# Kernel optimization log

Measured on AMD Instinct MI355X. Metric: run time of the kernel, lower is better.

Reference implementation:

```python
import jax, jax.numpy as jnp
import numpy as np

BAND_WIDTH = 0.05
EPS = 1e-5
NORM_EPS = 1e-12  # F.normalize clamp_min


def _l2_normalize_channels(x):
    # x: (B, C, D, H, W); normalize over channel dim=1 like F.normalize(p=2, dim=1)
    n = jnp.sqrt(jnp.sum(x * x, axis=1, keepdims=True))
    return x / jnp.maximum(n, NORM_EPS)


def setup_inputs() -> dict:
    key = jax.random.key(0)
    k1, k2, k3 = jax.random.split(key, 3)
    B, C, D, H, W = 2, 256, 8, 8, 8
    P, K = 128, 512  # n_patches iterations, k=512 sampled voxels per patch
    S = D * H * W  # 512 spatial voxels
    t2_feat = jax.random.normal(k1, (B, C, D, H, W), dtype=jnp.float32)
    t1_feat = jax.random.normal(k2, (B, C, D, H, W), dtype=jnp.float32)
    idx = jax.random.randint(k3, (P, K), 0, S, dtype=jnp.int32)
    return {"t2_feat": t2_feat, "t1_feat": t1_feat, "idx": idx}


def reference(t2_feat, t1_feat, idx):
    B, C = t2_feat.shape[:2]
    # normalize channels, flatten spatial dims: (B, C, S)
    t2 = _l2_normalize_channels(t2_feat).reshape(B, C, -1)
    t1 = _l2_normalize_channels(t1_feat).reshape(B, C, -1)
    # gather the same random voxels for both modalities: (B, C, P, K)
    t2p = t2[:, :, idx]
    t1p = t1[:, :, idx]
    # batched cosine similarity: bmm(t2p^T, t1p) per patch -> (P, B, K, K)
    cs = jnp.einsum('bcpk,bcpl->pbkl', t2p, t1p)
    e = jnp.exp(cs / BAND_WIDTH)
    pos = jnp.diagonal(e, axis1=2, axis2=3)  # (P, B, K) exp of positives
    # InfoNCE over columns (torch dim=1 of (B,K,K)) and rows (dim=2)
    info_nce1 = pos / jnp.sum(e, axis=2)
    info_nce2 = pos / jnp.sum(e, axis=3)
    info_nce = 0.5 * (info_nce1 + info_nce2)
    # per-patch mean of -log, then mean over patches == global mean
    return jnp.mean(-jnp.log(info_nce + EPS))
```

## Files before the change

kernel.cpp:

```cpp
#include <hip/hip_runtime.h>

typedef __attribute__((ext_vector_type(8))) short bf16x8;
typedef __attribute__((ext_vector_type(4))) float f32x4;
typedef __attribute__((ext_vector_type(4))) ushort u16x4;

#define C_DIM 256
#define S_DIM 512
#define P_DIM 128
#define K_DIM 512
#define INV_BW 20.0f
#define EPS_LOSS 1e-5f

#define OFF_SS2    0
#define OFF_SS1    1024
#define OFF_DIAG   2048
#define OFF_CNTBF  3072
#define OFF_T2BF   35840
#define OFF_T1BF   166912
#define OFF_EBF    297984
#define OFF_ETBF   560128
#define OFF_D1P    35840
#define OFF_D2P    822272
#define OFF_PART   1084416
#define OFF_TICKET 1084544

__device__ inline ushort f2bf(float f) {
  union { float f; uint u; } v; v.f = f;
  return (ushort)((v.u + 0x7FFF + ((v.u >> 16) & 1)) >> 16);
}

#define TP 260
__global__ __launch_bounds__(256) void pre_kernel(
    const float* __restrict__ t2, const float* __restrict__ t1,
    const int* __restrict__ idx,
    float* __restrict__ ss2, float* __restrict__ ss1,
    ushort* __restrict__ t2bfT, ushort* __restrict__ t1bfT,
    ushort* __restrict__ cntbf, int* __restrict__ ticket) {
  int blk = blockIdx.x, tid = threadIdx.x;
  if (blk < 64) {
    __shared__ ushort tl[16][TP];
    __shared__ float ps[16][17];
    int b = blk >> 5, stile = blk & 31;
    int s0 = stile * 16;
    int ls = tid & 15, cg = tid >> 4;
    int wv = tid >> 6, ln = tid & 63;
    #pragma unroll
    for (int tt = 0; tt < 2; ++tt) {
      const float* src = (tt ? t1 : t2) + b * (C_DIM * S_DIM);
      ushort* dst = (tt ? t1bfT : t2bfT) + b * (S_DIM * C_DIM);
      float a = 0.f;
      #pragma unroll
      for (int k = 0; k < 16; ++k) {
        int c = cg + 16 * k;
        float v = src[c * S_DIM + s0 + ls];
        a += v * v;
        tl[ls][c] = f2bf(v);
      }
      ps[cg][ls] = a;
      __syncthreads();
      if (tid < 16) {
        float ss = 0.f;
        #pragma unroll
        for (int j = 0; j < 16; ++j) ss += ps[j][tid];
        (tt ? ss1 : ss2)[b * S_DIM + s0 + tid] = ss;
      }
      #pragma unroll
      for (int i = 0; i < 4; ++i) {
        int sl = wv * 4 + i;
        u16x4 pk = *reinterpret_cast<const u16x4*>(&tl[sl][ln * 4]);
        *reinterpret_cast<u16x4*>(&dst[(s0 + sl) * C_DIM + ln * 4]) = pk;
      }
      __syncthreads();
    }
  } else {
    __shared__ int c_lds[S_DIM];
    int p = blk - 64;
    if (blk == 64 && tid == 0) *ticket = 0;
    c_lds[tid] = 0; c_lds[tid + 256] = 0;
    __syncthreads();
    atomicAdd(&c_lds[idx[p * K_DIM + tid]], 1);
    atomicAdd(&c_lds[idx[p * K_DIM + tid + 256]], 1);
    __syncthreads();
    cntbf[p * S_DIM + tid]       = f2bf((float)c_lds[tid]);
    cntbf[p * S_DIM + tid + 256] = f2bf((float)c_lds[tid + 256]);
  }
}

__global__ __launch_bounds__(256) void gemm_exp_mfma_kernel(
    const ushort* __restrict__ t2bfT, const ushort* __restrict__ t1bfT,
    const float* __restrict__ ss2, const float* __restrict__ ss1,
    ushort* __restrict__ Ebf, ushort* __restrict__ ETbf,
    float* __restrict__ diag) {
  int wave = threadIdx.x >> 6, lane = threadIdx.x & 63;
  int job = blockIdx.x * 4 + wave;
  int n = job & 31, m = (job >> 5) & 31, b = job >> 10;
  int m0 = m * 16, c0 = n * 16;
  int lr = lane & 15, lo = lane >> 4;
  const ushort* ap = t2bfT + b * (S_DIM * C_DIM) + (m0 + lr) * C_DIM + lo * 8;
  const ushort* bp = t1bfT + b * (S_DIM * C_DIM) + (c0 + lr) * C_DIM + lo * 8;
  f32x4 acc = {0.f, 0.f, 0.f, 0.f};
  #pragma unroll
  for (int k = 0; k < 8; ++k) {
    bf16x8 af = *reinterpret_cast<const bf16x8*>(ap + k * 32);
    bf16x8 bv = *reinterpret_cast<const bf16x8*>(bp + k * 32);
    acc = __builtin_amdgcn_mfma_f32_16x16x32_bf16(af, bv, acc, 0, 0, 0);
  }
  float bs = 1.0f / fmaxf(sqrtf(ss1[b * S_DIM + c0 + lr]), 1e-12f);
  float e[4]; ushort eb[4];
  ushort* Eb  = Ebf  + b * (S_DIM * S_DIM);
  ushort* ETb = ETbf + b * (S_DIM * S_DIM);
  #pragma unroll
  for (int r = 0; r < 4; ++r) {
    int row = m0 + lo * 4 + r;
    float as = 1.0f / fmaxf(sqrtf(ss2[b * S_DIM + row]), 1e-12f);
    e[r] = expf(acc[r] * as * bs * INV_BW);
    eb[r] = f2bf(e[r]);
    Eb[row * S_DIM + c0 + lr] = eb[r];
  }
  u16x4 pk = {eb[0], eb[1], eb[2], eb[3]};
  *reinterpret_cast<u16x4*>(&ETb[(c0 + lr) * S_DIM + m0 + lo * 4]) = pk;
  if (m == n && (lr >> 2) == lo) diag[b * S_DIM + m0 + lr] = e[lr & 3];
}

__global__ __launch_bounds__(256) void denom_mfma_kernel(
    const ushort* __restrict__ Ebf, const ushort* __restrict__ ETbf,
    const ushort* __restrict__ cntbf,
    float* __restrict__ D1p, float* __restrict__ D2p) {
  int wave = threadIdx.x >> 6, lane = threadIdx.x & 63;
  int job = blockIdx.x * 4 + wave;
  int n = job & 31, m = (job >> 5) & 7, b = (job >> 8) & 1;
  int z = (job >> 9) & 1, h = job >> 10;
  int m0 = m * 16, col0 = n * 16;
  const ushort* Bmat = (z ? Ebf : ETbf) + b * (S_DIM * S_DIM);
  float* Dp = (z ? D2p : D1p) + h * (P_DIM * 2 * S_DIM);
  int lr = lane & 15, lo = lane >> 4;
  const ushort* aptr = cntbf + (m0 + lr) * S_DIM + h * 256 + lo * 8;
  const ushort* bptr = Bmat + (col0 + lr) * S_DIM + h * 256 + lo * 8;
  f32x4 acc = {0.f, 0.f, 0.f, 0.f};
  #pragma unroll
  for (int k = 0; k < 8; ++k) {
    bf16x8 af = *reinterpret_cast<const bf16x8*>(aptr + k * 32);
    bf16x8 bv = *reinterpret_cast<const bf16x8*>(bptr + k * 32);
    acc = __builtin_amdgcn_mfma_f32_16x16x32_bf16(af, bv, acc, 0, 0, 0);
  }
  #pragma unroll
  for (int r = 0; r < 4; ++r) {
    int p = m0 + lo * 4 + r;
    Dp[(p * 2 + b) * S_DIM + col0 + lr] = acc[r];
  }
}

__global__ __launch_bounds__(512) void loss_final_kernel(
    const int* __restrict__ idx, const float* __restrict__ diag,
    const float* __restrict__ D1p, const float* __restrict__ D2p,
    float* __restrict__ part, int* __restrict__ ticket, float* __restrict__ out) {
  const int HOFF = P_DIM * 2 * S_DIM;
  int p = blockIdx.x, k = threadIdx.x;
  int s = idx[p * K_DIM + k];
  float acc = 0.f;
  #pragma unroll
  for (int b = 0; b < 2; ++b) {
    float pos = diag[b * S_DIM + s];
    int o = (p * 2 + b) * S_DIM + s;
    float d1 = D1p[o] + D1p[HOFF + o];
    float d2 = D2p[o] + D2p[HOFF + o];
    acc += logf(0.5f * (pos / d1 + pos / d2) + EPS_LOSS);
  }
  for (int o = 32; o; o >>= 1) acc += __shfl_down(acc, o);
  __shared__ float red[8];
  __shared__ int lastflag;
  if ((k & 63) == 0) red[k >> 6] = acc;
  __syncthreads();
  if (k == 0) {
    float tsum = 0.f;
    #pragma unroll
    for (int i = 0; i < 8; ++i) tsum += red[i];
    atomicExch(&part[p], tsum);
    __threadfence();
    int old = atomicAdd(ticket, 1);
    lastflag = (old == P_DIM - 1);
  }
  __syncthreads();
  if (lastflag) {
    __threadfence();
    float v = (k < P_DIM) ? atomicAdd(&part[k], 0.0f) : 0.0f;
    for (int o = 32; o; o >>= 1) v += __shfl_down(v, o);
    __shared__ float red2[8];
    if ((k & 63) == 0) red2[k >> 6] = v;
    __syncthreads();
    if (k == 0) {
      float tsum = 0.f;
      #pragma unroll
      for (int i = 0; i < 8; ++i) tsum += red2[i];
      out[0] = -tsum * (1.0f / (P_DIM * 2.0f * K_DIM));
    }
  }
}

extern "C" void kernel_launch(void* const* d_in, const int* in_sizes, int n_in,
                              void* d_out, int out_size, void* d_ws, size_t ws_size,
                              hipStream_t stream) {
  const float* t2 = (const float*)d_in[0];
  const float* t1 = (const float*)d_in[1];
  const int* idx  = (const int*)d_in[2];
  float* ws = (float*)d_ws;
  float*  ss2    = ws + OFF_SS2;
  float*  ss1    = ws + OFF_SS1;
  float*  diag   = ws + OFF_DIAG;
  ushort* cntbf  = (ushort*)(ws + OFF_CNTBF);
  ushort* t2bfT  = (ushort*)(ws + OFF_T2BF);
  ushort* t1bfT  = (ushort*)(ws + OFF_T1BF);
  ushort* Ebf    = (ushort*)(ws + OFF_EBF);
  ushort* ETbf   = (ushort*)(ws + OFF_ETBF);
  float*  D1p    = ws + OFF_D1P;
  float*  D2p    = ws + OFF_D2P;
  float*  part   = ws + OFF_PART;
  int*    ticket = (int*)(ws + OFF_TICKET);

  pre_kernel<<<192, 256, 0, stream>>>(t2, t1, idx, ss2, ss1, t2bfT, t1bfT,
                                      cntbf, ticket);
  gemm_exp_mfma_kernel<<<512, 256, 0, stream>>>(t2bfT, t1bfT, ss2, ss1,
                                                Ebf, ETbf, diag);
  denom_mfma_kernel<<<512, 256, 0, stream>>>(Ebf, ETbf, cntbf, D1p, D2p);
  loss_final_kernel<<<P_DIM, 512, 0, stream>>>(idx, diag, D1p, D2p, part, ticket,
                                               (float*)d_out);
}
```

Baseline: 30.66 us.

## Fuse Gram/exp and count-weighted denominator GEMMs into one kernel via LDS

Merges the exp-Gram kernel and the denominator GEMM into a single kernel. Each block computes a 16-column strip of exp(similarity) for one side, holds it in LDS as bf16, then immediately multiplies it by the patch count matrix to produce full-K denominators. This removes the global round trip of the 512x512 E and E^T matrices, one kernel launch, and the half-split partial sums. The pre-kernel is also split so each block handles one tensor, doubling its parallelism. In exchange the fused kernel runs only 128 blocks with 512 threads, which may underfill the GPU, and each side recomputes its own Gram strip.

Measured after the change: 34.36 us. 1.12x slower.

```diff
diff --git a/kernel.cpp b/kernel.cpp
--- a/kernel.cpp
+++ b/kernel.cpp
@@ -17,12 +17,10 @@
 #define OFF_CNTBF  3072
 #define OFF_T2BF   35840
 #define OFF_T1BF   166912
-#define OFF_EBF    297984
-#define OFF_ETBF   560128
-#define OFF_D1P    35840
-#define OFF_D2P    822272
-#define OFF_PART   1084416
-#define OFF_TICKET 1084544
+#define OFF_D1     297984
+#define OFF_D2     429056
+#define OFF_PART   560128
+#define OFF_TICKET 560256
 
 __device__ inline ushort f2bf(float f) {
   union { float f; uint u; } v; v.f = f;
@@ -37,45 +35,42 @@
     ushort* __restrict__ t2bfT, ushort* __restrict__ t1bfT,
     ushort* __restrict__ cntbf, int* __restrict__ ticket) {
   int blk = blockIdx.x, tid = threadIdx.x;
-  if (blk < 64) {
+  if (blk < 128) {
     __shared__ ushort tl[16][TP];
     __shared__ float ps[16][17];
-    int b = blk >> 5, stile = blk & 31;
+    int tt = blk >> 6, b = (blk >> 5) & 1, stile = blk & 31;
     int s0 = stile * 16;
+    const float* src = (tt ? t1 : t2) + b * (C_DIM * S_DIM);
+    ushort* dst = (tt ? t1bfT : t2bfT) + b * (S_DIM * C_DIM);
+    float* ssd = (tt ? ss1 : ss2) + b * S_DIM;
     int ls = tid & 15, cg = tid >> 4;
+    float a = 0.f;
+    #pragma unroll
+    for (int k = 0; k < 16; ++k) {
+      int c = cg + 16 * k;
+      float v = src[c * S_DIM + s0 + ls];
+      a += v * v;
+      tl[ls][c] = f2bf(v);
+    }
+    ps[cg][ls] = a;
+    __syncthreads();
+    if (tid < 16) {
+      float ss = 0.f;
+      #pragma unroll
+      for (int j = 0; j < 16; ++j) ss += ps[j][tid];
+      ssd[s0 + tid] = ss;
+    }
     int wv = tid >> 6, ln = tid & 63;
     #pragma unroll
-    for (int tt = 0; tt < 2; ++tt) {
-      const float* src = (tt ? t1 : t2) + b * (C_DIM * S_DIM);
-      ushort* dst = (tt ? t1bfT : t2bfT) + b * (S_DIM * C_DIM);
-      float a = 0.f;
-      #pragma unroll
-      for (int k = 0; k < 16; ++k) {
-        int c = cg + 16 * k;
-        float v = src[c * S_DIM + s0 + ls];
-        a += v * v;
-        tl[ls][c] = f2bf(v);
-      }
-      ps[cg][ls] = a;
-      __syncthreads();
-      if (tid < 16) {
-        float ss = 0.f;
-        #pragma unroll
-        for (int j = 0; j < 16; ++j) ss += ps[j][tid];
-        (tt ? ss1 : ss2)[b * S_DIM + s0 + tid] = ss;
-      }
-      #pragma unroll
-      for (int i = 0; i < 4; ++i) {
-        int sl = wv * 4 + i;
-        u16x4 pk = *reinterpret_cast<const u16x4*>(&tl[sl][ln * 4]);
-        *reinterpret_cast<u16x4*>(&dst[(s0 + sl) * C_DIM + ln * 4]) = pk;
-      }
-      __syncthreads();
+    for (int i = 0; i < 4; ++i) {
+      int sl = wv * 4 + i;
+      u16x4 pk = *reinterpret_cast<const u16x4*>(&tl[sl][ln * 4]);
+      *reinterpret_cast<u16x4*>(&dst[(s0 + sl) * C_DIM + ln * 4]) = pk;
     }
   } else {
     __shared__ int c_lds[S_DIM];
-    int p = blk - 64;
-    if (blk == 64 && tid == 0) *ticket = 0;
+    int p = blk - 128;
+    if (blk == 128 && tid == 0) *ticket = 0;
     c_lds[tid] = 0; c_lds[tid + 256] = 0;
     __syncthreads();
     atomicAdd(&c_lds[idx[p * K_DIM + tid]], 1);
@@ -86,75 +81,71 @@
   }
 }
 
-__global__ __launch_bounds__(256) void gemm_exp_mfma_kernel(
+__global__ __launch_bounds__(512) void gram_denom_kernel(
     const ushort* __restrict__ t2bfT, const ushort* __restrict__ t1bfT,
     const float* __restrict__ ss2, const float* __restrict__ ss1,
-    ushort* __restrict__ Ebf, ushort* __restrict__ ETbf,
-    float* __restrict__ diag) {
+    const ushort* __restrict__ cntbf,
+    float* __restrict__ D1, float* __restrict__ D2, float* __restrict__ diag) {
+  __shared__ ushort ldsE[16][520];
+  int blk = blockIdx.x;
+  int side = blk >> 6, b = (blk >> 5) & 1, fb = blk & 31;
+  int f0 = fb * 16;
   int wave = threadIdx.x >> 6, lane = threadIdx.x & 63;
-  int job = blockIdx.x * 4 + wave;
-  int n = job & 31, m = (job >> 5) & 31, b = job >> 10;
-  int m0 = m * 16, c0 = n * 16;
   int lr = lane & 15, lo = lane >> 4;
-  const ushort* ap = t2bfT + b * (S_DIM * C_DIM) + (m0 + lr) * C_DIM + lo * 8;
-  const ushort* bp = t1bfT + b * (S_DIM * C_DIM) + (c0 + lr) * C_DIM + lo * 8;
+  const ushort* varMat = (side ? t1bfT : t2bfT) + b * (S_DIM * C_DIM);
+  const ushort* fixMat = (side ? t2bfT : t1bfT) + b * (S_DIM * C_DIM);
+  const float* vss = (side ? ss1 : ss2) + b * S_DIM;
+  const float* fss = (side ? ss2 : ss1) + b * S_DIM;
+  float fscale = 1.0f / fmaxf(sqrtf(fss[f0 + lr]), 1e-12f);
+  bf16x8 ffr[8];
+  #pragma unroll
+  for (int k = 0; k < 8; ++k)
+    ffr[k] = *reinterpret_cast<const bf16x8*>(
+        fixMat + (f0 + lr) * C_DIM + lo * 8 + k * 32);
+  #pragma unroll
+  for (int i = 0; i < 4; ++i) {
+    int v0 = (wave * 4 + i) * 16;
+    const ushort* ap = varMat + (v0 + lr) * C_DIM + lo * 8;
+    f32x4 acc = {0.f, 0.f, 0.f, 0.f};
+    #pragma unroll
+    for (int k = 0; k < 8; ++k) {
+      bf16x8 af = *reinterpret_cast<const bf16x8*>(ap + k * 32);
+      acc = __builtin_amdgcn_mfma_f32_16x16x32_bf16(af, ffr[k], acc, 0, 0, 0);
+    }
+    ushort eb[4];
+    #pragma unroll
+    for (int r = 0; r < 4; ++r) {
+      int vrow = v0 + lo * 4 + r;
+      float vs = 1.0f / fmaxf(sqrtf(vss[vrow]), 1e-12f);
+      float e = expf(acc[r] * vs * fscale * INV_BW);
+      eb[r] = f2bf(e);
+      if (side == 0 && vrow == f0 + lr) diag[b * S_DIM + vrow] = e;
+    }
+    u16x4 pk = {eb[0], eb[1], eb[2], eb[3]};
+    *reinterpret_cast<u16x4*>(&ldsE[lr][v0 + lo * 4]) = pk;
+  }
+  __syncthreads();
+  int p0 = wave * 16;
+  const ushort* cp = cntbf + (p0 + lr) * S_DIM + lo * 8;
   f32x4 acc = {0.f, 0.f, 0.f, 0.f};
   #pragma unroll
-  for (int k = 0; k < 8; ++k) {
-    bf16x8 af = *reinterpret_cast<const bf16x8*>(ap + k * 32);
-    bf16x8 bv = *reinterpret_cast<const bf16x8*>(bp + k * 32);
-    acc = __builtin_amdgcn_mfma_f32_16x16x32_bf16(af, bv, acc, 0, 0, 0);
-  }
-  float bs = 1.0f / fmaxf(sqrtf(ss1[b * S_DIM + c0 + lr]), 1e-12f);
-  float e[4]; ushort eb[4];
-  ushort* Eb  = Ebf  + b * (S_DIM * S_DIM);
-  ushort* ETb = ETbf + b * (S_DIM * S_DIM);
+  for (int k = 0; k < 16; ++k) {
+    bf16x8 af = *reinterpret_cast<const bf16x8*>(cp + k * 32);
+    bf16x8 bf_ = *reinterpret_cast<const bf16x8*>(&ldsE[lr][lo * 8 + k * 32]);
+    acc = __builtin_amdgcn_mfma_f32_16x16x32_bf16(af, bf_, acc, 0, 0, 0);
+  }
+  float* Dout = side ? D2 : D1;
   #pragma unroll
   for (int r = 0; r < 4; ++r) {
-    int row = m0 + lo * 4 + r;
-    float as = 1.0f / fmaxf(sqrtf(ss2[b * S_DIM + row]), 1e-12f);
-    e[r] = expf(acc[r] * as * bs * INV_BW);
-    eb[r] = f2bf(e[r]);
-    Eb[row * S_DIM + c0 + lr] = eb[r];
-  }
-  u16x4 pk = {eb[0], eb[1], eb[2], eb[3]};
-  *reinterpret_cast<u16x4*>(&ETb[(c0 + lr) * S_DIM + m0 + lo * 4]) = pk;
-  if (m == n && (lr >> 2) == lo) diag[b * S_DIM + m0 + lr] = e[lr & 3];
-}
-
-__global__ __launch_bounds__(256) void denom_mfma_kernel(
-    const ushort* __restrict__ Ebf, const ushort* __restrict__ ETbf,
-    const ushort* __restrict__ cntbf,
-    float* __restrict__ D1p, float* __restrict__ D2p) {
-  int wave = threadIdx.x >> 6, lane = threadIdx.x & 63;
-  int job = blockIdx.x * 4 + wave;
-  int n = job & 31, m = (job >> 5) & 7, b = (job >> 8) & 1;
-  int z = (job >> 9) & 1, h = job >> 10;
-  int m0 = m * 16, col0 = n * 16;
-  const ushort* Bmat = (z ? Ebf : ETbf) + b * (S_DIM * S_DIM);
-  float* Dp = (z ? D2p : D1p) + h * (P_DIM * 2 * S_DIM);
-  int lr = lane & 15, lo = lane >> 4;
-  const ushort* aptr = cntbf + (m0 + lr) * S_DIM + h * 256 + lo * 8;
-  const ushort* bptr = Bmat + (col0 + lr) * S_DIM + h * 256 + lo * 8;
-  f32x4 acc = {0.f, 0.f, 0.f, 0.f};
-  #pragma unroll
-  for (int k = 0; k < 8; ++k) {
-    bf16x8 af = *reinterpret_cast<const bf16x8*>(aptr + k * 32);
-    bf16x8 bv = *reinterpret_cast<const bf16x8*>(bptr + k * 32);
-    acc = __builtin_amdgcn_mfma_f32_16x16x32_bf16(af, bv, acc, 0, 0, 0);
-  }
-  #pragma unroll
-  for (int r = 0; r < 4; ++r) {
-    int p = m0 + lo * 4 + r;
-    Dp[(p * 2 + b) * S_DIM + col0 + lr] = acc[r];
+    int p = p0 + lo * 4 + r;
+    Dout[(p * 2 + b) * S_DIM + f0 + lr] = acc[r];
   }
 }
 
 __global__ __launch_bounds__(512) void loss_final_kernel(
     const int* __restrict__ idx, const float* __restrict__ diag,
-    const float* __restrict__ D1p, const float* __restrict__ D2p,
+    const float* __restrict__ D1, const float* __restrict__ D2,
     float* __restrict__ part, int* __restrict__ ticket, float* __restrict__ out) {
-  const int HOFF = P_DIM * 2 * S_DIM;
   int p = blockIdx.x, k = threadIdx.x;
   int s = idx[p * K_DIM + k];
   float acc = 0.f;
@@ -162,8 +153,8 @@
   for (int b = 0; b < 2; ++b) {
     float pos = diag[b * S_DIM + s];
     int o = (p * 2 + b) * S_DIM + s;
-    float d1 = D1p[o] + D1p[HOFF + o];
-    float d2 = D2p[o] + D2p[HOFF + o];
+    float d1 = D1[o];
+    float d2 = D2[o];
     acc += logf(0.5f * (pos / d1 + pos / d2) + EPS_LOSS);
   }
   for (int o = 32; o; o >>= 1) acc += __shfl_down(acc, o);
@@ -210,18 +201,15 @@
   ushort* cntbf  = (ushort*)(ws + OFF_CNTBF);
   ushort* t2bfT  = (ushort*)(ws + OFF_T2BF);
   ushort* t1bfT  = (ushort*)(ws + OFF_T1BF);
-  ushort* Ebf    = (ushort*)(ws + OFF_EBF);
-  ushort* ETbf   = (ushort*)(ws + OFF_ETBF);
-  float*  D1p    = ws + OFF_D1P;
-  float*  D2p    = ws + OFF_D2P;
+  float*  D1     = ws + OFF_D1;
+  float*  D2     = ws + OFF_D2;
   float*  part   = ws + OFF_PART;
   int*    ticket = (int*)(ws + OFF_TICKET);
 
-  pre_kernel<<<192, 256, 0, stream>>>(t2, t1, idx, ss2, ss1, t2bfT, t1bfT,
+  pre_kernel<<<256, 256, 0, stream>>>(t2, t1, idx, ss2, ss1, t2bfT, t1bfT,
                                       cntbf, ticket);
-  gemm_exp_mfma_kernel<<<512, 256, 0, stream>>>(t2bfT, t1bfT, ss2, ss1,
-                                                Ebf, ETbf, diag);
-  denom_mfma_kernel<<<512, 256, 0, stream>>>(Ebf, ETbf, cntbf, D1p, D2p);
-  loss_final_kernel<<<P_DIM, 512, 0, stream>>>(idx, diag, D1p, D2p, part, ticket,
+  gram_denom_kernel<<<128, 512, 0, stream>>>(t2bfT, t1bfT, ss2, ss1, cntbf,
+                                             D1, D2, diag);
+  loss_final_kernel<<<P_DIM, 512, 0, stream>>>(idx, diag, D1, D2, part, ticket,
                                                (float*)d_out);
 }
```

## Fuse gemm, denominator and loss kernels into one persistent kernel with grid barriers

Applied to the files above, without the earlier changes.

Merges the three post-processing kernels into a single 256-block, 512-thread kernel that separates the GEMM+exp, denominator GEMM and loss stages with software grid barriers built on agent-scope atomics. It also splits the pre-kernel so each block converts one tensor instead of two, giving 256 blocks. The aim is to remove two kernel launch gaps. The cost is spin-wait barriers that depend on all 256 blocks being co-resident, and D buffers moved to new workspace offsets.

Measured after the change: 54.08 us. 76.4% more time.

```diff
diff --git a/kernel.cpp b/kernel.cpp
--- a/kernel.cpp
+++ b/kernel.cpp
@@ -19,14 +19,26 @@
 #define OFF_T1BF   166912
 #define OFF_EBF    297984
 #define OFF_ETBF   560128
-#define OFF_D1P    35840
-#define OFF_D2P    822272
-#define OFF_PART   1084416
-#define OFF_TICKET 1084544
+#define OFF_D1     822272
+#define OFF_D2     1084416
+#define OFF_PART   1346560
+#define OFF_BAR    1346816
 
 __device__ inline ushort f2bf(float f) {
   union { float f; uint u; } v; v.f = f;
   return (ushort)((v.u + 0x7FFF + ((v.u >> 16) & 1)) >> 16);
+}
+
+__device__ inline void grid_barrier(int* c, int n) {
+  __syncthreads();
+  if (threadIdx.x == 0) {
+    __builtin_amdgcn_fence(__ATOMIC_RELEASE, "agent");
+    __hip_atomic_fetch_add(c, 1, __ATOMIC_RELAXED, __HIP_MEMORY_SCOPE_AGENT);
+    while (__hip_atomic_load(c, __ATOMIC_RELAXED, __HIP_MEMORY_SCOPE_AGENT) < n)
+      __builtin_amdgcn_s_sleep(2);
+    __builtin_amdgcn_fence(__ATOMIC_ACQUIRE, "agent");
+  }
+  __syncthreads();
 }
 
 #define TP 260
@@ -35,47 +47,44 @@
     const int* __restrict__ idx,
     float* __restrict__ ss2, float* __restrict__ ss1,
     ushort* __restrict__ t2bfT, ushort* __restrict__ t1bfT,
-    ushort* __restrict__ cntbf, int* __restrict__ ticket) {
+    ushort* __restrict__ cntbf, int* __restrict__ bar) {
   int blk = blockIdx.x, tid = threadIdx.x;
-  if (blk < 64) {
+  if (blk < 128) {
     __shared__ ushort tl[16][TP];
     __shared__ float ps[16][17];
-    int b = blk >> 5, stile = blk & 31;
+    int tt = blk >> 6, b = (blk >> 5) & 1, stile = blk & 31;
     int s0 = stile * 16;
+    const float* src = (tt ? t1 : t2) + b * (C_DIM * S_DIM);
+    ushort* dst = (tt ? t1bfT : t2bfT) + b * (S_DIM * C_DIM);
+    float* ssd = (tt ? ss1 : ss2) + b * S_DIM;
     int ls = tid & 15, cg = tid >> 4;
+    float a = 0.f;
+    #pragma unroll
+    for (int k = 0; k < 16; ++k) {
+      int c = cg + 16 * k;
+      float v = src[c * S_DIM + s0 + ls];
+      a += v * v;
+      tl[ls][c] = f2bf(v);
+    }
+    ps[cg][ls] = a;
+    __syncthreads();
+    if (tid < 16) {
+      float ss = 0.f;
+      #pragma unroll
+      for (int j = 0; j < 16; ++j) ss += ps[j][tid];
+      ssd[s0 + tid] = ss;
+    }
     int wv = tid >> 6, ln = tid & 63;
     #pragma unroll
-    for (int tt = 0; tt < 2; ++tt) {
-      const float* src = (tt ? t1 : t2) + b * (C_DIM * S_DIM);
-      ushort* dst = (tt ? t1bfT : t2bfT) + b * (S_DIM * C_DIM);
-      float a = 0.f;
-      #pragma unroll
-      for (int k = 0; k < 16; ++k) {
-        int c = cg + 16 * k;
-        float v = src[c * S_DIM + s0 + ls];
-        a += v * v;
-        tl[ls][c] = f2bf(v);
-      }
-      ps[cg][ls] = a;
-      __syncthreads();
-      if (tid < 16) {
-        float ss = 0.f;
-        #pragma unroll
-        for (int j = 0; j < 16; ++j) ss += ps[j][tid];
-        (tt ? ss1 : ss2)[b * S_DIM + s0 + tid] = ss;
-      }
-      #pragma unroll
-      for (int i = 0; i < 4; ++i) {
-        int sl = wv * 4 + i;
-        u16x4 pk = *reinterpret_cast<const u16x4*>(&tl[sl][ln * 4]);
-        *reinterpret_cast<u16x4*>(&dst[(s0 + sl) * C_DIM + ln * 4]) = pk;
-      }
-      __syncthreads();
+    for (int i = 0; i < 4; ++i) {
+      int sl = wv * 4 + i;
+      u16x4 pk = *reinterpret_cast<const u16x4*>(&tl[sl][ln * 4]);
+      *reinterpret_cast<u16x4*>(&dst[(s0 + sl) * C_DIM + ln * 4]) = pk;
     }
   } else {
     __shared__ int c_lds[S_DIM];
-    int p = blk - 64;
-    if (blk == 64 && tid == 0) *ticket = 0;
+    int p = blk - 128;
+    if (blk == 128 && tid < 3) bar[tid] = 0;
     c_lds[tid] = 0; c_lds[tid + 256] = 0;
     __syncthreads();
     atomicAdd(&c_lds[idx[p * K_DIM + tid]], 1);
@@ -86,113 +95,114 @@
   }
 }
 
-__global__ __launch_bounds__(256) void gemm_exp_mfma_kernel(
+__global__ __launch_bounds__(512) void fused_kernel(
     const ushort* __restrict__ t2bfT, const ushort* __restrict__ t1bfT,
     const float* __restrict__ ss2, const float* __restrict__ ss1,
+    const ushort* __restrict__ cntbf, const int* __restrict__ idx,
     ushort* __restrict__ Ebf, ushort* __restrict__ ETbf,
-    float* __restrict__ diag) {
-  int wave = threadIdx.x >> 6, lane = threadIdx.x & 63;
-  int job = blockIdx.x * 4 + wave;
-  int n = job & 31, m = (job >> 5) & 31, b = job >> 10;
-  int m0 = m * 16, c0 = n * 16;
+    float* __restrict__ D1, float* __restrict__ D2, float* __restrict__ diag,
+    float* __restrict__ part2, int* __restrict__ bar, float* __restrict__ out) {
+  int blk = blockIdx.x, tid = threadIdx.x;
+  int wave = tid >> 6, lane = tid & 63;
   int lr = lane & 15, lo = lane >> 4;
-  const ushort* ap = t2bfT + b * (S_DIM * C_DIM) + (m0 + lr) * C_DIM + lo * 8;
-  const ushort* bp = t1bfT + b * (S_DIM * C_DIM) + (c0 + lr) * C_DIM + lo * 8;
-  f32x4 acc = {0.f, 0.f, 0.f, 0.f};
-  #pragma unroll
-  for (int k = 0; k < 8; ++k) {
-    bf16x8 af = *reinterpret_cast<const bf16x8*>(ap + k * 32);
-    bf16x8 bv = *reinterpret_cast<const bf16x8*>(bp + k * 32);
-    acc = __builtin_amdgcn_mfma_f32_16x16x32_bf16(af, bv, acc, 0, 0, 0);
-  }
-  float bs = 1.0f / fmaxf(sqrtf(ss1[b * S_DIM + c0 + lr]), 1e-12f);
-  float e[4]; ushort eb[4];
-  ushort* Eb  = Ebf  + b * (S_DIM * S_DIM);
-  ushort* ETb = ETbf + b * (S_DIM * S_DIM);
-  #pragma unroll
-  for (int r = 0; r < 4; ++r) {
-    int row = m0 + lo * 4 + r;
-    float as = 1.0f / fmaxf(sqrtf(ss2[b * S_DIM + row]), 1e-12f);
-    e[r] = expf(acc[r] * as * bs * INV_BW);
-    eb[r] = f2bf(e[r]);
-    Eb[row * S_DIM + c0 + lr] = eb[r];
-  }
-  u16x4 pk = {eb[0], eb[1], eb[2], eb[3]};
-  *reinterpret_cast<u16x4*>(&ETb[(c0 + lr) * S_DIM + m0 + lo * 4]) = pk;
-  if (m == n && (lr >> 2) == lo) diag[b * S_DIM + m0 + lr] = e[lr & 3];
-}
-
-__global__ __launch_bounds__(256) void denom_mfma_kernel(
-    const ushort* __restrict__ Ebf, const ushort* __restrict__ ETbf,
-    const ushort* __restrict__ cntbf,
-    float* __restrict__ D1p, float* __restrict__ D2p) {
-  int wave = threadIdx.x >> 6, lane = threadIdx.x & 63;
-  int job = blockIdx.x * 4 + wave;
-  int n = job & 31, m = (job >> 5) & 7, b = (job >> 8) & 1;
-  int z = (job >> 9) & 1, h = job >> 10;
-  int m0 = m * 16, col0 = n * 16;
-  const ushort* Bmat = (z ? Ebf : ETbf) + b * (S_DIM * S_DIM);
-  float* Dp = (z ? D2p : D1p) + h * (P_DIM * 2 * S_DIM);
-  int lr = lane & 15, lo = lane >> 4;
-  const ushort* aptr = cntbf + (m0 + lr) * S_DIM + h * 256 + lo * 8;
-  const ushort* bptr = Bmat + (col0 + lr) * S_DIM + h * 256 + lo * 8;
-  f32x4 acc = {0.f, 0.f, 0.f, 0.f};
-  #pragma unroll
-  for (int k = 0; k < 8; ++k) {
-    bf16x8 af = *reinterpret_cast<const bf16x8*>(aptr + k * 32);
-    bf16x8 bv = *reinterpret_cast<const bf16x8*>(bptr + k * 32);
-    acc = __builtin_amdgcn_mfma_f32_16x16x32_bf16(af, bv, acc, 0, 0, 0);
-  }
-  #pragma unroll
-  for (int r = 0; r < 4; ++r) {
-    int p = m0 + lo * 4 + r;
-    Dp[(p * 2 + b) * S_DIM + col0 + lr] = acc[r];
-  }
-}
-
-__global__ __launch_bounds__(512) void loss_final_kernel(
-    const int* __restrict__ idx, const float* __restrict__ diag,
-    const float* __restrict__ D1p, const float* __restrict__ D2p,
-    float* __restrict__ part, int* __restrict__ ticket, float* __restrict__ out) {
-  const int HOFF = P_DIM * 2 * S_DIM;
-  int p = blockIdx.x, k = threadIdx.x;
-  int s = idx[p * K_DIM + k];
-  float acc = 0.f;
-  #pragma unroll
-  for (int b = 0; b < 2; ++b) {
+
+  {
+    int job = blk * 8 + wave;
+    int n = job & 31, m = (job >> 5) & 31, b = job >> 10;
+    int m0 = m * 16, c0 = n * 16;
+    const ushort* ap = t2bfT + b * (S_DIM * C_DIM) + (m0 + lr) * C_DIM + lo * 8;
+    const ushort* bp = t1bfT + b * (S_DIM * C_DIM) + (c0 + lr) * C_DIM + lo * 8;
+    f32x4 acc = {0.f, 0.f, 0.f, 0.f};
+    #pragma unroll
+    for (int k = 0; k < 8; ++k) {
+      bf16x8 af = *reinterpret_cast<const bf16x8*>(ap + k * 32);
+      bf16x8 bv = *reinterpret_cast<const bf16x8*>(bp + k * 32);
+      acc = __builtin_amdgcn_mfma_f32_16x16x32_bf16(af, bv, acc, 0, 0, 0);
+    }
+    float bs = 1.0f / fmaxf(sqrtf(ss1[b * S_DIM + c0 + lr]), 1e-12f);
+    float e[4]; ushort eb[4];
+    ushort* Eb  = Ebf  + b * (S_DIM * S_DIM);
+    ushort* ETb = ETbf + b * (S_DIM * S_DIM);
+    #pragma unroll
+    for (int r = 0; r < 4; ++r) {
+      int row = m0 + lo * 4 + r;
+      float as = 1.0f / fmaxf(sqrtf(ss2[b * S_DIM + row]), 1e-12f);
+      e[r] = expf(acc[r] * as * bs * INV_BW);
+      eb[r] = f2bf(e[r]);
+      Eb[row * S_DIM + c0 + lr] = eb[r];
+    }
+    u16x4 pk = {eb[0], eb[1], eb[2], eb[3]};
+    *reinterpret_cast<u16x4*>(&ETb[(c0 + lr) * S_DIM + m0 + lo * 4]) = pk;
+    if (m == n && (lr >> 2) == lo) diag[b * S_DIM + m0 + lr] = e[lr & 3];
+  }
+  grid_barrier(&bar[0], 256);
+
+  {
+    int job = blk * 8 + wave;
+    int n = job & 31, m = (job >> 5) & 7, b = (job >> 8) & 1;
+    int z = (job >> 9) & 1, h = job >> 10;
+    int m0 = m * 16, col0 = n * 16;
+    const ushort* Bmat = (z ? Ebf : ETbf) + b * (S_DIM * S_DIM);
+    const ushort* aptr = cntbf + (m0 + lr) * S_DIM + h * 256 + lo * 8;
+    const ushort* bptr = Bmat + (col0 + lr) * S_DIM + h * 256 + lo * 8;
+    f32x4 acc = {0.f, 0.f, 0.f, 0.f};
+    #pragma unroll
+    for (int k = 0; k < 8; ++k) {
+      bf16x8 af = *reinterpret_cast<const bf16x8*>(aptr + k * 32);
+      bf16x8 bv = *reinterpret_cast<const bf16x8*>(bptr + k * 32);
+      acc = __builtin_amdgcn_mfma_f32_16x16x32_bf16(af, bv, acc, 0, 0, 0);
+    }
+    float* Dp = (z ? D2 : D1);
+    #pragma unroll
+    for (int r = 0; r < 4; ++r) {
+      int p = m0 + lo * 4 + r;
+      Dp[((h * P_DIM + p) * 2 + b) * S_DIM + col0 + lr] = acc[r];
+    }
+  }
+  grid_barrier(&bar[1], 256);
+
+  {
+    const int HOFF = P_DIM * 2 * S_DIM;
+    int p = blk >> 1, kh = blk & 1;
+    int b = tid >> 8, kk = kh * 256 + (tid & 255);
+    int s = idx[p * K_DIM + kk];
     float pos = diag[b * S_DIM + s];
     int o = (p * 2 + b) * S_DIM + s;
-    float d1 = D1p[o] + D1p[HOFF + o];
-    float d2 = D2p[o] + D2p[HOFF + o];
-    acc += logf(0.5f * (pos / d1 + pos / d2) + EPS_LOSS);
-  }
-  for (int o = 32; o; o >>= 1) acc += __shfl_down(acc, o);
-  __shared__ float red[8];
-  __shared__ int lastflag;
-  if ((k & 63) == 0) red[k >> 6] = acc;
-  __syncthreads();
-  if (k == 0) {
-    float tsum = 0.f;
-    #pragma unroll
-    for (int i = 0; i < 8; ++i) tsum += red[i];
-    atomicExch(&part[p], tsum);
-    __threadfence();
-    int old = atomicAdd(ticket, 1);
-    lastflag = (old == P_DIM - 1);
-  }
-  __syncthreads();
-  if (lastflag) {
-    __threadfence();
-    float v = (k < P_DIM) ? atomicAdd(&part[k], 0.0f) : 0.0f;
-    for (int o = 32; o; o >>= 1) v += __shfl_down(v, o);
-    __shared__ float red2[8];
-    if ((k & 63) == 0) red2[k >> 6] = v;
-    __syncthreads();
-    if (k == 0) {
+    float d1 = D1[o] + D1[HOFF + o];
+    float d2 = D2[o] + D2[HOFF + o];
+    float term = logf(0.5f * (pos / d1 + pos / d2) + EPS_LOSS);
+    for (int off = 32; off; off >>= 1) term += __shfl_down(term, off);
+    __shared__ float red[8];
+    __shared__ int lastflag;
+    if (lane == 0) red[wave] = term;
+    __syncthreads();
+    if (tid == 0) {
       float tsum = 0.f;
       #pragma unroll
-      for (int i = 0; i < 8; ++i) tsum += red2[i];
-      out[0] = -tsum * (1.0f / (P_DIM * 2.0f * K_DIM));
+      for (int i = 0; i < 8; ++i) tsum += red[i];
+      atomicExch(&part2[blk], tsum);
+      __builtin_amdgcn_fence(__ATOMIC_RELEASE, "agent");
+      int old = __hip_atomic_fetch_add(&bar[2], 1, __ATOMIC_ACQ_REL,
+                                       __HIP_MEMORY_SCOPE_AGENT);
+      lastflag = (old == 255);
+    }
+    __syncthreads();
+    if (lastflag) {
+      if (tid == 0) __builtin_amdgcn_fence(__ATOMIC_ACQUIRE, "agent");
+      __syncthreads();
+      float v = (tid < 256)
+          ? __hip_atomic_load(&part2[tid], __ATOMIC_RELAXED,
+                              __HIP_MEMORY_SCOPE_AGENT) : 0.f;
+      for (int off = 32; off; off >>= 1) v += __shfl_down(v, off);
+      __shared__ float red2[8];
+      if (lane == 0) red2[wave] = v;
+      __syncthreads();
+      if (tid == 0) {
+        float tsum = 0.f;
+        #pragma unroll
+        for (int i = 0; i < 8; ++i) tsum += red2[i];
+        out[0] = -tsum * (1.0f / (P_DIM * 2.0f * K_DIM));
+      }
     }
   }
 }
@@ -212,16 +222,14 @@
   ushort* t1bfT  = (ushort*)(ws + OFF_T1BF);
   ushort* Ebf    = (ushort*)(ws + OFF_EBF);
   ushort* ETbf   = (ushort*)(ws + OFF_ETBF);
-  float*  D1p    = ws + OFF_D1P;
-  float*  D2p    = ws + OFF_D2P;
-  float*  part   = ws + OFF_PART;
-  int*    ticket = (int*)(ws + OFF_TICKET);
-
-  pre_kernel<<<192, 256, 0, stream>>>(t2, t1, idx, ss2, ss1, t2bfT, t1bfT,
-                                      cntbf, ticket);
-  gemm_exp_mfma_kernel<<<512, 256, 0, stream>>>(t2bfT, t1bfT, ss2, ss1,
-                                                Ebf, ETbf, diag);
-  denom_mfma_kernel<<<512, 256, 0, stream>>>(Ebf, ETbf, cntbf, D1p, D2p);
-  loss_final_kernel<<<P_DIM, 512, 0, stream>>>(idx, diag, D1p, D2p, part, ticket,
-                                               (float*)d_out);
-}
+  float*  D1     = ws + OFF_D1;
+  float*  D2     = ws + OFF_D2;
+  float*  part2  = ws + OFF_PART;
+  int*    bar    = (int*)(ws + OFF_BAR);
+
+  pre_kernel<<<256, 256, 0, stream>>>(t2, t1, idx, ss2, ss1, t2bfT, t1bfT,
+                                      cntbf, bar);
+  fused_kernel<<<256, 512, 0, stream>>>(t2bfT, t1bfT, ss2, ss1, cntbf, idx,
+                                        Ebf, ETbf, D1, D2, diag, part2, bar,
+                                        (float*)d_out);
+}
```

## Reuse MFMA operand fragments across two tiles per wave and split pre-kernel work

Applied to the files above, without the earlier changes.

Each wave in the GEMM-exp and denominator kernels now keeps one operand's fragments in registers and computes two 16x16 output tiles, halving those kernels' grid sizes and cutting redundant global loads. The pre-kernel splits the t2/t1 conversion across twice as many blocks instead of looping in one block. It also uses fast __expf/__logf intrinsics and moves the D1/D2 buffers to their own workspace region rather than overlapping the bf16 transposes. The trade-off is fewer waves available to hide latency and slightly lower precision from the fast math.

New measurement: 30.08 us. About the same (-1.9%).

```diff
diff --git a/kernel.cpp b/kernel.cpp
--- a/kernel.cpp
+++ b/kernel.cpp
@@ -19,10 +19,10 @@
 #define OFF_T1BF   166912
 #define OFF_EBF    297984
 #define OFF_ETBF   560128
-#define OFF_D1P    35840
-#define OFF_D2P    822272
-#define OFF_PART   1084416
-#define OFF_TICKET 1084544
+#define OFF_D1     822272
+#define OFF_D2     1084416
+#define OFF_PART   1346560
+#define OFF_BAR    1346816
 
 __device__ inline ushort f2bf(float f) {
   union { float f; uint u; } v; v.f = f;
@@ -35,47 +35,44 @@
     const int* __restrict__ idx,
     float* __restrict__ ss2, float* __restrict__ ss1,
     ushort* __restrict__ t2bfT, ushort* __restrict__ t1bfT,
-    ushort* __restrict__ cntbf, int* __restrict__ ticket) {
+    ushort* __restrict__ cntbf, int* __restrict__ bar) {
   int blk = blockIdx.x, tid = threadIdx.x;
-  if (blk < 64) {
+  if (blk < 128) {
     __shared__ ushort tl[16][TP];
     __shared__ float ps[16][17];
-    int b = blk >> 5, stile = blk & 31;
+    int tt = blk >> 6, b = (blk >> 5) & 1, stile = blk & 31;
     int s0 = stile * 16;
+    const float* src = (tt ? t1 : t2) + b * (C_DIM * S_DIM);
+    ushort* dst = (tt ? t1bfT : t2bfT) + b * (S_DIM * C_DIM);
+    float* ssd = (tt ? ss1 : ss2) + b * S_DIM;
     int ls = tid & 15, cg = tid >> 4;
+    float a = 0.f;
+    #pragma unroll
+    for (int k = 0; k < 16; ++k) {
+      int c = cg + 16 * k;
+      float v = src[c * S_DIM + s0 + ls];
+      a += v * v;
+      tl[ls][c] = f2bf(v);
+    }
+    ps[cg][ls] = a;
+    __syncthreads();
+    if (tid < 16) {
+      float ss = 0.f;
+      #pragma unroll
+      for (int j = 0; j < 16; ++j) ss += ps[j][tid];
+      ssd[s0 + tid] = ss;
+    }
     int wv = tid >> 6, ln = tid & 63;
     #pragma unroll
-    for (int tt = 0; tt < 2; ++tt) {
-      const float* src = (tt ? t1 : t2) + b * (C_DIM * S_DIM);
-      ushort* dst = (tt ? t1bfT : t2bfT) + b * (S_DIM * C_DIM);
-      float a = 0.f;
-      #pragma unroll
-      for (int k = 0; k < 16; ++k) {
-        int c = cg + 16 * k;
-        float v = src[c * S_DIM + s0 + ls];
-        a += v * v;
-        tl[ls][c] = f2bf(v);
-      }
-      ps[cg][ls] = a;
-      __syncthreads();
-      if (tid < 16) {
-        float ss = 0.f;
-        #pragma unroll
-        for (int j = 0; j < 16; ++j) ss += ps[j][tid];
-        (tt ? ss1 : ss2)[b * S_DIM + s0 + tid] = ss;
-      }
-      #pragma unroll
-      for (int i = 0; i < 4; ++i) {
-        int sl = wv * 4 + i;
-        u16x4 pk = *reinterpret_cast<const u16x4*>(&tl[sl][ln * 4]);
-        *reinterpret_cast<u16x4*>(&dst[(s0 + sl) * C_DIM + ln * 4]) = pk;
-      }
-      __syncthreads();
+    for (int i = 0; i < 4; ++i) {
+      int sl = wv * 4 + i;
+      u16x4 pk = *reinterpret_cast<const u16x4*>(&tl[sl][ln * 4]);
+      *reinterpret_cast<u16x4*>(&dst[(s0 + sl) * C_DIM + ln * 4]) = pk;
     }
   } else {
     __shared__ int c_lds[S_DIM];
-    int p = blk - 64;
-    if (blk == 64 && tid == 0) *ticket = 0;
+    int p = blk - 128;
+    if (blk == 128 && tid < 3) bar[tid] = 0;
     c_lds[tid] = 0; c_lds[tid + 256] = 0;
     __syncthreads();
     atomicAdd(&c_lds[idx[p * K_DIM + tid]], 1);
@@ -93,67 +90,82 @@
     float* __restrict__ diag) {
   int wave = threadIdx.x >> 6, lane = threadIdx.x & 63;
   int job = blockIdx.x * 4 + wave;
-  int n = job & 31, m = (job >> 5) & 31, b = job >> 10;
-  int m0 = m * 16, c0 = n * 16;
+  int n = job & 31, mp = (job >> 5) & 15, b = job >> 9;
+  int c0 = n * 16;
   int lr = lane & 15, lo = lane >> 4;
-  const ushort* ap = t2bfT + b * (S_DIM * C_DIM) + (m0 + lr) * C_DIM + lo * 8;
+  const ushort* base2 = t2bfT + b * (S_DIM * C_DIM);
   const ushort* bp = t1bfT + b * (S_DIM * C_DIM) + (c0 + lr) * C_DIM + lo * 8;
-  f32x4 acc = {0.f, 0.f, 0.f, 0.f};
-  #pragma unroll
-  for (int k = 0; k < 8; ++k) {
-    bf16x8 af = *reinterpret_cast<const bf16x8*>(ap + k * 32);
-    bf16x8 bv = *reinterpret_cast<const bf16x8*>(bp + k * 32);
-    acc = __builtin_amdgcn_mfma_f32_16x16x32_bf16(af, bv, acc, 0, 0, 0);
-  }
+  bf16x8 bfr[8];
+  #pragma unroll
+  for (int k = 0; k < 8; ++k)
+    bfr[k] = *reinterpret_cast<const bf16x8*>(bp + k * 32);
   float bs = 1.0f / fmaxf(sqrtf(ss1[b * S_DIM + c0 + lr]), 1e-12f);
-  float e[4]; ushort eb[4];
   ushort* Eb  = Ebf  + b * (S_DIM * S_DIM);
   ushort* ETb = ETbf + b * (S_DIM * S_DIM);
   #pragma unroll
-  for (int r = 0; r < 4; ++r) {
-    int row = m0 + lo * 4 + r;
-    float as = 1.0f / fmaxf(sqrtf(ss2[b * S_DIM + row]), 1e-12f);
-    e[r] = expf(acc[r] * as * bs * INV_BW);
-    eb[r] = f2bf(e[r]);
-    Eb[row * S_DIM + c0 + lr] = eb[r];
-  }
-  u16x4 pk = {eb[0], eb[1], eb[2], eb[3]};
-  *reinterpret_cast<u16x4*>(&ETb[(c0 + lr) * S_DIM + m0 + lo * 4]) = pk;
-  if (m == n && (lr >> 2) == lo) diag[b * S_DIM + m0 + lr] = e[lr & 3];
+  for (int t = 0; t < 2; ++t) {
+    int m0 = mp * 32 + t * 16;
+    const ushort* ap = base2 + (m0 + lr) * C_DIM + lo * 8;
+    f32x4 acc = {0.f, 0.f, 0.f, 0.f};
+    #pragma unroll
+    for (int k = 0; k < 8; ++k) {
+      bf16x8 af = *reinterpret_cast<const bf16x8*>(ap + k * 32);
+      acc = __builtin_amdgcn_mfma_f32_16x16x32_bf16(af, bfr[k], acc, 0, 0, 0);
+    }
+    float e[4]; ushort eb[4];
+    #pragma unroll
+    for (int r = 0; r < 4; ++r) {
+      int row = m0 + lo * 4 + r;
+      float as = 1.0f / fmaxf(sqrtf(ss2[b * S_DIM + row]), 1e-12f);
+      e[r] = __expf(acc[r] * as * bs * INV_BW);
+      eb[r] = f2bf(e[r]);
+      Eb[row * S_DIM + c0 + lr] = eb[r];
+    }
+    u16x4 pk = {eb[0], eb[1], eb[2], eb[3]};
+    *reinterpret_cast<u16x4*>(&ETb[(c0 + lr) * S_DIM + m0 + lo * 4]) = pk;
+    if (m0 == c0 && (lr >> 2) == lo) diag[b * S_DIM + m0 + lr] = e[lr & 3];
+  }
 }
 
 __global__ __launch_bounds__(256) void denom_mfma_kernel(
     const ushort* __restrict__ Ebf, const ushort* __restrict__ ETbf,
     const ushort* __restrict__ cntbf,
-    float* __restrict__ D1p, float* __restrict__ D2p) {
+    float* __restrict__ D1, float* __restrict__ D2) {
   int wave = threadIdx.x >> 6, lane = threadIdx.x & 63;
   int job = blockIdx.x * 4 + wave;
-  int n = job & 31, m = (job >> 5) & 7, b = (job >> 8) & 1;
-  int z = (job >> 9) & 1, h = job >> 10;
-  int m0 = m * 16, col0 = n * 16;
+  int np = job & 15, m = (job >> 4) & 7, b = (job >> 7) & 1;
+  int z = (job >> 8) & 1, h = job >> 9;
+  int m0 = m * 16;
+  int lr = lane & 15, lo = lane >> 4;
   const ushort* Bmat = (z ? Ebf : ETbf) + b * (S_DIM * S_DIM);
-  float* Dp = (z ? D2p : D1p) + h * (P_DIM * 2 * S_DIM);
-  int lr = lane & 15, lo = lane >> 4;
+  float* Dp = (z ? D2 : D1);
   const ushort* aptr = cntbf + (m0 + lr) * S_DIM + h * 256 + lo * 8;
-  const ushort* bptr = Bmat + (col0 + lr) * S_DIM + h * 256 + lo * 8;
-  f32x4 acc = {0.f, 0.f, 0.f, 0.f};
-  #pragma unroll
-  for (int k = 0; k < 8; ++k) {
-    bf16x8 af = *reinterpret_cast<const bf16x8*>(aptr + k * 32);
-    bf16x8 bv = *reinterpret_cast<const bf16x8*>(bptr + k * 32);
-    acc = __builtin_amdgcn_mfma_f32_16x16x32_bf16(af, bv, acc, 0, 0, 0);
-  }
-  #pragma unroll
-  for (int r = 0; r < 4; ++r) {
-    int p = m0 + lo * 4 + r;
-    Dp[(p * 2 + b) * S_DIM + col0 + lr] = acc[r];
+  bf16x8 afr[8];
+  #pragma unroll
+  for (int k = 0; k < 8; ++k)
+    afr[k] = *reinterpret_cast<const bf16x8*>(aptr + k * 32);
+  #pragma unroll
+  for (int t = 0; t < 2; ++t) {
+    int col0 = np * 32 + t * 16;
+    const ushort* bptr = Bmat + (col0 + lr) * S_DIM + h * 256 + lo * 8;
+    f32x4 acc = {0.f, 0.f, 0.f, 0.f};
+    #pragma unroll
+    for (int k = 0; k < 8; ++k) {
+      bf16x8 bv = *reinterpret_cast<const bf16x8*>(bptr + k * 32);
+      acc = __builtin_amdgcn_mfma_f32_16x16x32_bf16(afr[k], bv, acc, 0, 0, 0);
+    }
+    #pragma unroll
+    for (int r = 0; r < 4; ++r) {
+      int p = m0 + lo * 4 + r;
+      Dp[((h * P_DIM + p) * 2 + b) * S_DIM + col0 + lr] = acc[r];
+    }
   }
 }
 
 __global__ __launch_bounds__(512) void loss_final_kernel(
     const int* __restrict__ idx, const float* __restrict__ diag,
-    const float* __restrict__ D1p, const float* __restrict__ D2p,
-    float* __restrict__ part, int* __restrict__ ticket, float* __restrict__ out) {
+    const float* __restrict__ D1, const float* __restrict__ D2,
+    float* __restrict__ part, int* __restrict__ bar, float* __restrict__ out) {
   const int HOFF = P_DIM * 2 * S_DIM;
   int p = blockIdx.x, k = threadIdx.x;
   int s = idx[p * K_DIM + k];
@@ -162,9 +174,9 @@
   for (int b = 0; b < 2; ++b) {
     float pos = diag[b * S_DIM + s];
     int o = (p * 2 + b) * S_DIM + s;
-    float d1 = D1p[o] + D1p[HOFF + o];
-    float d2 = D2p[o] + D2p[HOFF + o];
-    acc += logf(0.5f * (pos / d1 + pos / d2) + EPS_LOSS);
+    float d1 = D1[o] + D1[HOFF + o];
+    float d2 = D2[o] + D2[HOFF + o];
+    acc += __logf(0.5f * (pos / d1 + pos / d2) + EPS_LOSS);
   }
   for (int o = 32; o; o >>= 1) acc += __shfl_down(acc, o);
   __shared__ float red[8];
@@ -177,7 +189,7 @@
     for (int i = 0; i < 8; ++i) tsum += red[i];
     atomicExch(&part[p], tsum);
     __threadfence();
-    int old = atomicAdd(ticket, 1);
+    int old = atomicAdd(&bar[2], 1);
     lastflag = (old == P_DIM - 1);
   }
   __syncthreads();
@@ -212,16 +224,16 @@
   ushort* t1bfT  = (ushort*)(ws + OFF_T1BF);
   ushort* Ebf    = (ushort*)(ws + OFF_EBF);
   ushort* ETbf   = (ushort*)(ws + OFF_ETBF);
-  float*  D1p    = ws + OFF_D1P;
-  float*  D2p    = ws + OFF_D2P;
+  float*  D1     = ws + OFF_D1;
+  float*  D2     = ws + OFF_D2;
   float*  part   = ws + OFF_PART;
-  int*    ticket = (int*)(ws + OFF_TICKET);
-
-  pre_kernel<<<192, 256, 0, stream>>>(t2, t1, idx, ss2, ss1, t2bfT, t1bfT,
-                                      cntbf, ticket);
-  gemm_exp_mfma_kernel<<<512, 256, 0, stream>>>(t2bfT, t1bfT, ss2, ss1,
+  int*    bar    = (int*)(ws + OFF_BAR);
+
+  pre_kernel<<<256, 256, 0, stream>>>(t2, t1, idx, ss2, ss1, t2bfT, t1bfT,
+                                      cntbf, bar);
+  gemm_exp_mfma_kernel<<<256, 256, 0, stream>>>(t2bfT, t1bfT, ss2, ss1,
                                                 Ebf, ETbf, diag);
-  denom_mfma_kernel<<<512, 256, 0, stream>>>(Ebf, ETbf, cntbf, D1p, D2p);
-  loss_final_kernel<<<P_DIM, 512, 0, stream>>>(idx, diag, D1p, D2p, part, ticket,
+  denom_mfma_kernel<<<256, 256, 0, stream>>>(Ebf, ETbf, cntbf, D1, D2);
+  loss_final_kernel<<<P_DIM, 512, 0, stream>>>(idx, diag, D1, D2, part, bar,
                                                (float*)d_out);
 }
```
